# Optimization experiments

Measured on AMD Instinct MI355X. Metric: run time of the kernel, lower is better.

Reference implementation:

```python
import jax, jax.numpy as jnp
import numpy as np

DIM = 1024
B, S = 4, 4096

def setup_inputs() -> dict:
    key = jax.random.key(0)
    ks = jax.random.split(key, 8)
    scale = 1.0 / np.sqrt(DIM)
    x = jax.random.normal(ks[0], (B, S, DIM), dtype=jnp.float32)
    Wk = jax.random.normal(ks[1], (DIM, DIM), dtype=jnp.float32) * scale
    Wv = jax.random.normal(ks[2], (DIM, DIM), dtype=jnp.float32) * scale
    Wr = jax.random.normal(ks[3], (DIM, DIM), dtype=jnp.float32) * scale
    Wo = jax.random.normal(ks[4], (DIM, DIM), dtype=jnp.float32) * scale
    time_decay = jax.random.normal(ks[5], (DIM,), dtype=jnp.float32) * 0.01 - 5.0
    time_first = jax.random.normal(ks[6], (DIM,), dtype=jnp.float32) * 0.01
    return {"x": x, "Wk": Wk, "Wv": Wv, "Wr": Wr, "Wo": Wo,
            "time_decay": time_decay, "time_first": time_first}

def reference(x, Wk, Wv, Wr, Wo, time_decay, time_first):
    # Projections (Linear with weight [out, in]: y = x @ W^T)
    k = jnp.einsum('bsd,ed->bse', x, Wk)
    v = jnp.einsum('bsd,ed->bse', x, Wv)
    r = jax.nn.sigmoid(jnp.einsum('bsd,ed->bse', x, Wr))
    w = -jnp.exp(time_decay)          # (D,)
    decay = jnp.exp(w)                # exp(w), per-channel decay in (0,1)
    eu = jnp.exp(time_first)          # exp(u)
    kv = k * v                        # (B, S, D)

    def step(state, kv_t):
        wkv = state + eu * kv_t       # output numerator this step
        new_state = decay * state + kv_t
        return new_state, wkv

    state0 = jnp.zeros((x.shape[0], x.shape[2]), dtype=x.dtype)
    # scan over time axis: move S to leading dim
    _, wkv_seq = jax.lax.scan(step, state0, jnp.swapaxes(kv, 0, 1))  # (S, B, D)
    out = r * jnp.swapaxes(wkv_seq, 0, 1)  # (B, S, D)
    return jnp.einsum('bsd,ed->bse', out, Wo)
```

## Files before the change

kernel.cpp:

```cpp
#include <hip/hip_runtime.h>
#include <hip/hip_bf16.h>

#define DIMD   1024
#define BATCH  4
#define SEQ    4096
#define NTOK   (BATCH * SEQ)
#define CHUNK  64
#define NCHUNK (SEQ / CHUNK)

#define KBK    64
#define NKT    (DIMD / KBK)

typedef unsigned short ushort_t;
typedef __attribute__((ext_vector_type(8))) __bf16   bf16x8;
typedef __attribute__((ext_vector_type(4))) float    f32x4;
typedef __attribute__((ext_vector_type(8))) ushort_t u16x8;

__device__ __forceinline__ float b2f(ushort_t u) {
    union { unsigned int i; float f; } x;
    x.i = ((unsigned int)u) << 16;
    return x.f;
}

__device__ __forceinline__ ushort_t f2b(float f) {
    union { float f; unsigned int i; } x;
    x.f = f;
    unsigned int r = x.i + 0x7fffu + ((x.i >> 16) & 1u);
    return (ushort_t)(r >> 16);
}

#define GLL(gsrc, ldst) __builtin_amdgcn_global_load_lds( \
    (__attribute__((address_space(1))) void*)(gsrc), \
    (__attribute__((address_space(3))) void*)(ldst), 16, 0, 0)

__global__ __launch_bounds__(256)
void conv_f2b(const float* __restrict__ src, ushort_t* __restrict__ dst, int n8)
{
    const int i = blockIdx.x * 256 + threadIdx.x;
    if (i >= n8) return;
    const float4* s4 = (const float4*)src;
    const float4 a = s4[i * 2];
    const float4 b = s4[i * 2 + 1];
    u16x8 o;
    o[0] = f2b(a.x); o[1] = f2b(a.y); o[2] = f2b(a.z); o[3] = f2b(a.w);
    o[4] = f2b(b.x); o[5] = f2b(b.y); o[6] = f2b(b.z); o[7] = f2b(b.w);
    *(u16x8*)(dst + (size_t)i * 8) = o;
}

__global__ __launch_bounds__(256)
void conv_w(const float* __restrict__ W0, const float* __restrict__ W1,
            const float* __restrict__ W2, const float* __restrict__ W3,
            ushort_t* __restrict__ dst)
{
    const int m = blockIdx.y;
    const float* src = (m == 0) ? W0 : (m == 1) ? W1 : (m == 2) ? W2 : W3;
    const int i = blockIdx.x * 256 + threadIdx.x;
    const float4* s4 = (const float4*)src;
    const float4 a = s4[i * 2];
    const float4 b = s4[i * 2 + 1];
    u16x8 o;
    o[0] = f2b(a.x); o[1] = f2b(a.y); o[2] = f2b(a.z); o[3] = f2b(a.w);
    o[4] = f2b(b.x); o[5] = f2b(b.y); o[6] = f2b(b.z); o[7] = f2b(b.w);
    *(u16x8*)(dst + (size_t)m * DIMD * DIMD + (size_t)i * 8) = o;
}

__global__ __launch_bounds__(512, 2)
void gemm_kvr(const ushort_t* __restrict__ A,
              const ushort_t* __restrict__ Wk,
              const ushort_t* __restrict__ Wv,
              const ushort_t* __restrict__ Wr,
              const float* __restrict__ td,
              ushort_t* __restrict__ Okv,
              ushort_t* __restrict__ Or,
              float* __restrict__ cs)
{
    __shared__ __align__(16) ushort_t As[2][256 * KBK];
    __shared__ __align__(16) ushort_t Bk[2][64 * KBK];
    __shared__ __align__(16) ushort_t Bv[2][64 * KBK];
    __shared__ __align__(16) ushort_t Br[2][64 * KBK];

    const int tid  = threadIdx.x;
    const int lane = tid & 63;
    const int wv   = tid >> 6;
    const int wr   = wv >> 1;
    const int wc   = wv & 1;
    const int lrow = lane & 15;
    const int kq   = lane >> 4;
    const int s8   = lrow & 7;
    const int sw0  = (kq ^ s8) * 8;
    const int sw1  = ((kq + 4) ^ s8) * 8;

    const int row0 = blockIdx.x * 256;
    const int e0   = blockIdx.y * 64;

    const int r_  = tid >> 3;
    const int q_  = ((tid & 7) ^ (r_ & 7)) * 8;
    const size_t aoffs = (size_t)(row0 + r_) * DIMD + q_;
    const size_t boffs = (size_t)(e0 + r_) * DIMD + q_;

#define KVR_STAGE_A(dst, k0) do { \
    _Pragma("unroll") \
    for (int it_ = 0; it_ < 4; ++it_) \
        GLL(A + aoffs + (size_t)it_ * 64 * DIMD + (k0), \
            (char*)(dst) + (tid + it_ * 512) * 16); \
} while (0)

#define KVR_STAGE_B(dk, dv, dr, k0) do { \
    GLL(Wk + boffs + (k0), (char*)(dk) + tid * 16); \
    GLL(Wv + boffs + (k0), (char*)(dv) + tid * 16); \
    GLL(Wr + boffs + (k0), (char*)(dr) + tid * 16); \
} while (0)

    f32x4 ak[4][2], av[4][2], aR[4][2];
#pragma unroll
    for (int i = 0; i < 4; i++)
#pragma unroll
        for (int j = 0; j < 2; j++) {
            ak[i][j] = f32x4{0.f, 0.f, 0.f, 0.f};
            av[i][j] = f32x4{0.f, 0.f, 0.f, 0.f};
            aR[i][j] = f32x4{0.f, 0.f, 0.f, 0.f};
        }

    KVR_STAGE_A(&As[0][0], 0);
    KVR_STAGE_B(&Bk[0][0], &Bv[0][0], &Br[0][0], 0);
    asm volatile("" ::: "memory");
    KVR_STAGE_A(&As[1][0], KBK);
    asm volatile("s_waitcnt vmcnt(4)" ::: "memory");
    __builtin_amdgcn_s_barrier();

    auto tile = [&](int kt, ushort_t* Asb, ushort_t* Bkb, ushort_t* Bvb,
                    ushort_t* Brb, ushort_t* Bkn, ushort_t* Bvn, ushort_t* Brn) {
        bf16x8 af0[4], af1[4], b0[2], b1[2], c0[2], c1[2], d0[2], d1[2];

#pragma unroll
        for (int i = 0; i < 4; i++)
            af0[i] = *(const bf16x8*)(Asb + (wr * 64 + i * 16 + lrow) * KBK + sw0);
#pragma unroll
        for (int j = 0; j < 2; j++) {
            const int bo = (wc * 32 + j * 16 + lrow) * KBK + sw0;
            b0[j] = *(const bf16x8*)(Bkb + bo);
            c0[j] = *(const bf16x8*)(Bvb + bo);
        }
        if (kt + 1 < NKT) KVR_STAGE_B(Bkn, Bvn, Brn, (kt + 1) * KBK);
        __builtin_amdgcn_s_barrier();
        asm volatile("s_waitcnt lgkmcnt(0)" ::: "memory");
        __builtin_amdgcn_sched_barrier(0);
        __builtin_amdgcn_s_setprio(1);
#pragma unroll
        for (int i = 0; i < 4; i++)
#pragma unroll
            for (int j = 0; j < 2; j++) {
                ak[i][j] = __builtin_amdgcn_mfma_f32_16x16x32_bf16(af0[i], b0[j], ak[i][j], 0, 0, 0);
                av[i][j] = __builtin_amdgcn_mfma_f32_16x16x32_bf16(af0[i], c0[j], av[i][j], 0, 0, 0);
            }
        __builtin_amdgcn_s_setprio(0);
        __builtin_amdgcn_s_barrier();

#pragma unroll
        for (int j = 0; j < 2; j++)
            d0[j] = *(const bf16x8*)(Brb + (wc * 32 + j * 16 + lrow) * KBK + sw0);
#pragma unroll
        for (int i = 0; i < 4; i++)
            af1[i] = *(const bf16x8*)(Asb + (wr * 64 + i * 16 + lrow) * KBK + sw1);
        __builtin_amdgcn_s_barrier();
        asm volatile("s_waitcnt lgkmcnt(0)" ::: "memory");
        __builtin_amdgcn_sched_barrier(0);
        __builtin_amdgcn_s_setprio(1);
#pragma unroll
        for (int i = 0; i < 4; i++)
#pragma unroll
            for (int j = 0; j < 2; j++)
                aR[i][j] = __builtin_amdgcn_mfma_f32_16x16x32_bf16(af0[i], d0[j], aR[i][j], 0, 0, 0);
        __builtin_amdgcn_s_setprio(0);
        __builtin_amdgcn_s_barrier();

#pragma unroll
        for (int j = 0; j < 2; j++) {
            const int bo = (wc * 32 + j * 16 + lrow) * KBK + sw1;
            b1[j] = *(const bf16x8*)(Bkb + bo);
            c1[j] = *(const bf16x8*)(Bvb + bo);
        }
        if (kt + 2 < NKT) KVR_STAGE_A(Asb, (kt + 2) * KBK);
        __builtin_amdgcn_s_barrier();
        asm volatile("s_waitcnt lgkmcnt(0)" ::: "memory");
        __builtin_amdgcn_sched_barrier(0);
        __builtin_amdgcn_s_setprio(1);
#pragma unroll
        for (int i = 0; i < 4; i++)
#pragma unroll
            for (int j = 0; j < 2; j++) {
                ak[i][j] = __builtin_amdgcn_mfma_f32_16x16x32_bf16(af1[i], b1[j], ak[i][j], 0, 0, 0);
                av[i][j] = __builtin_amdgcn_mfma_f32_16x16x32_bf16(af1[i], c1[j], av[i][j], 0, 0, 0);
            }
        __builtin_amdgcn_s_setprio(0);
        __builtin_amdgcn_s_barrier();

#pragma unroll
        for (int j = 0; j < 2; j++)
            d1[j] = *(const bf16x8*)(Brb + (wc * 32 + j * 16 + lrow) * KBK + sw1);
        __builtin_amdgcn_s_barrier();
        asm volatile("s_waitcnt lgkmcnt(0)" ::: "memory");
        __builtin_amdgcn_sched_barrier(0);
        __builtin_amdgcn_s_setprio(1);
#pragma unroll
        for (int i = 0; i < 4; i++)
#pragma unroll
            for (int j = 0; j < 2; j++)
                aR[i][j] = __builtin_amdgcn_mfma_f32_16x16x32_bf16(af1[i], d1[j], aR[i][j], 0, 0, 0);
        __builtin_amdgcn_s_setprio(0);
        if (kt < NKT - 2)       asm volatile("s_waitcnt vmcnt(4)" ::: "memory");
        else if (kt == NKT - 2) asm volatile("s_waitcnt vmcnt(0)" ::: "memory");
        __builtin_amdgcn_s_barrier();
    };

    for (int m = 0; m < NKT / 2; ++m) {
        tile(2 * m,     &As[0][0], &Bk[0][0], &Bv[0][0], &Br[0][0],
                        &Bk[1][0], &Bv[1][0], &Br[1][0]);
        tile(2 * m + 1, &As[1][0], &Bk[1][0], &Bv[1][0], &Br[1][0],
                        &Bk[0][0], &Bv[0][0], &Br[0][0]);
    }

#pragma unroll
    for (int i = 0; i < 4; i++)
#pragma unroll
        for (int j = 0; j < 2; j++)
#pragma unroll
            for (int r = 0; r < 4; r++) {
                const int row = row0 + wr * 64 + i * 16 + kq * 4 + r;
                const int col = e0 + wc * 32 + j * 16 + lrow;
                const size_t o = (size_t)row * DIMD + col;
                Okv[o] = f2b(ak[i][j][r] * av[i][j][r]);
                Or[o]  = f2b(1.f / (1.f + __expf(-aR[i][j][r])));
            }

#pragma unroll
    for (int j = 0; j < 2; j++) {
        const int col = e0 + wc * 32 + j * 16 + lrow;
        const float w = -__expf(td[col]);
        float s = 0.f;
#pragma unroll
        for (int i = 0; i < 4; i++)
#pragma unroll
            for (int r = 0; r < 4; r++) {
                const int rl = i * 16 + kq * 4 + r;
                s += __expf(w * (float)(63 - rl)) * ak[i][j][r] * av[i][j][r];
            }
        s += __shfl_xor(s, 16);
        s += __shfl_xor(s, 32);
        if (kq == 0) {
            const int gchunk = (row0 >> 6) + wr;
            cs[(size_t)gchunk * DIMD + col] = s;
        }
    }
#undef KVR_STAGE_A
#undef KVR_STAGE_B
}

__global__ __launch_bounds__(512, 2)
void gemm_bt(const ushort_t* __restrict__ A,
             const ushort_t* __restrict__ W,
             float* __restrict__ Of)
{
    __shared__ __align__(16) ushort_t As[2][256 * KBK];
    __shared__ __align__(16) ushort_t Bs[2][256 * KBK];

    const int tid  = threadIdx.x;
    const int lane = tid & 63;
    const int wv   = tid >> 6;
    const int wr   = wv >> 2;
    const int wc   = wv & 3;
    const int lrow = lane & 15;
    const int kq   = lane >> 4;
    const int s8   = lrow & 7;
    const int sw0  = (kq ^ s8) * 8;
    const int sw1  = ((kq + 4) ^ s8) * 8;

    const int row0 = blockIdx.x * 256;
    const int e0   = blockIdx.y * 256;

    const int r_  = tid >> 3;
    const int q_  = ((tid & 7) ^ (r_ & 7)) * 8;
    const size_t aoffs = (size_t)(row0 + r_) * DIMD + q_;
    const size_t boffs = (size_t)(e0 + r_) * DIMD + q_;

#define BT_STAGE_A(dst, k0) do { \
    _Pragma("unroll") \
    for (int it_ = 0; it_ < 4; ++it_) \
        GLL(A + aoffs + (size_t)it_ * 64 * DIMD + (k0), \
            (char*)(dst) + (tid + it_ * 512) * 16); \
} while (0)

#define BT_STAGE_B(dst, k0) do { \
    _Pragma("unroll") \
    for (int it_ = 0; it_ < 4; ++it_) \
        GLL(W + boffs + (size_t)it_ * 64 * DIMD + (k0), \
            (char*)(dst) + (tid + it_ * 512) * 16); \
} while (0)

    f32x4 acc[8][4];
#pragma unroll
    for (int i = 0; i < 8; i++)
#pragma unroll
        for (int j = 0; j < 4; j++)
            acc[i][j] = f32x4{0.f, 0.f, 0.f, 0.f};

    BT_STAGE_A(&As[0][0], 0);
    BT_STAGE_B(&Bs[0][0], 0);
    asm volatile("" ::: "memory");
    BT_STAGE_A(&As[1][0], KBK);
    asm volatile("s_waitcnt vmcnt(4)" ::: "memory");
    __builtin_amdgcn_s_barrier();

    auto tile = [&](int kt, ushort_t* Asb, ushort_t* Bsb, ushort_t* Bsn) {
        bf16x8 af0[8], af1[8], bf0[4], bf1[4];

#pragma unroll
        for (int i = 0; i < 8; i++)
            af0[i] = *(const bf16x8*)(Asb + (wr * 128 + i * 16 + lrow) * KBK + sw0);
#pragma unroll
        for (int j = 0; j < 2; j++)
            bf0[j] = *(const bf16x8*)(Bsb + (wc * 64 + j * 16 + lrow) * KBK + sw0);
        if (kt + 1 < NKT) BT_STAGE_B(Bsn, (kt + 1) * KBK);
        __builtin_amdgcn_s_barrier();
        asm volatile("s_waitcnt lgkmcnt(0)" ::: "memory");
        __builtin_amdgcn_sched_barrier(0);
        __builtin_amdgcn_s_setprio(1);
#pragma unroll
        for (int i = 0; i < 8; i++)
#pragma unroll
            for (int j = 0; j < 2; j++)
                acc[i][j] = __builtin_amdgcn_mfma_f32_16x16x32_bf16(af0[i], bf0[j], acc[i][j], 0, 0, 0);
        __builtin_amdgcn_s_setprio(0);
        __builtin_amdgcn_s_barrier();

#pragma unroll
        for (int j = 2; j < 4; j++)
            bf0[j] = *(const bf16x8*)(Bsb + (wc * 64 + j * 16 + lrow) * KBK + sw0);
        __builtin_amdgcn_s_barrier();
        asm volatile("s_waitcnt lgkmcnt(0)" ::: "memory");
        __builtin_amdgcn_sched_barrier(0);
        __builtin_amdgcn_s_setprio(1);
#pragma unroll
        for (int i = 0; i < 8; i++)
#pragma unroll
            for (int j = 2; j < 4; j++)
                acc[i][j] = __builtin_amdgcn_mfma_f32_16x16x32_bf16(af0[i], bf0[j], acc[i][j], 0, 0, 0);
        __builtin_amdgcn_s_setprio(0);
        __builtin_amdgcn_s_barrier();

#pragma unroll
        for (int i = 0; i < 8; i++)
            af1[i] = *(const bf16x8*)(Asb + (wr * 128 + i * 16 + lrow) * KBK + sw1);
#pragma unroll
        for (int j = 0; j < 2; j++)
            bf1[j] = *(const bf16x8*)(Bsb + (wc * 64 + j * 16 + lrow) * KBK + sw1);
        __builtin_amdgcn_s_barrier();
        asm volatile("s_waitcnt lgkmcnt(0)" ::: "memory");
        __builtin_amdgcn_sched_barrier(0);
        __builtin_amdgcn_s_setprio(1);
#pragma unroll
        for (int i = 0; i < 8; i++)
#pragma unroll
            for (int j = 0; j < 2; j++)
                acc[i][j] = __builtin_amdgcn_mfma_f32_16x16x32_bf16(af1[i], bf1[j], acc[i][j], 0, 0, 0);
        __builtin_amdgcn_s_setprio(0);
        __builtin_amdgcn_s_barrier();

#pragma unroll
        for (int j = 2; j < 4; j++)
            bf1[j] = *(const bf16x8*)(Bsb + (wc * 64 + j * 16 + lrow) * KBK + sw1);
        if (kt + 2 < NKT) BT_STAGE_A(Asb, (kt + 2) * KBK);
        __builtin_amdgcn_s_barrier();
        asm volatile("s_waitcnt lgkmcnt(0)" ::: "memory");
        __builtin_amdgcn_sched_barrier(0);
        __builtin_amdgcn_s_setprio(1);
#pragma unroll
        for (int i = 0; i < 8; i++)
#pragma unroll
            for (int j = 2; j < 4; j++)
                acc[i][j] = __builtin_amdgcn_mfma_f32_16x16x32_bf16(af1[i], bf1[j], acc[i][j], 0, 0, 0);
        __builtin_amdgcn_s_setprio(0);
        if (kt < NKT - 2)       asm volatile("s_waitcnt vmcnt(4)" ::: "memory");
        else if (kt == NKT - 2) asm volatile("s_waitcnt vmcnt(0)" ::: "memory");
        __builtin_amdgcn_s_barrier();
    };

    for (int m = 0; m < NKT / 2; ++m) {
        tile(2 * m,     &As[0][0], &Bs[0][0], &Bs[1][0]);
        tile(2 * m + 1, &As[1][0], &Bs[1][0], &Bs[0][0]);
    }

#pragma unroll
    for (int i = 0; i < 8; i++)
#pragma unroll
        for (int j = 0; j < 4; j++)
#pragma unroll
            for (int r = 0; r < 4; r++) {
                const int row = row0 + wr * 128 + i * 16 + kq * 4 + r;
                const int col = e0 + wc * 64 + j * 16 + lrow;
                Of[(size_t)row * DIMD + col] = acc[i][j][r];
            }
#undef BT_STAGE_A
#undef BT_STAGE_B
}

__global__ __launch_bounds__(64)
void chunk_scan(float* __restrict__ cs, const float* __restrict__ td)
{
    const int idx = blockIdx.x * 64 + threadIdx.x;
    const int d = idx & (DIMD - 1);
    const int b = idx >> 10;

    const float w      = -__expf(td[d]);
    const float decayL = __expf(w * (float)CHUNK);

    float v[NCHUNK];
    const size_t base = ((size_t)b * NCHUNK) * DIMD + d;
#pragma unroll
    for (int c = 0; c < NCHUNK; c++)
        v[c] = cs[base + (size_t)c * DIMD];

    float st = 0.f;
#pragma unroll
    for (int c = 0; c < NCHUNK; c++) {
        const float sc = v[c];
        v[c] = st;
        st = decayL * st + sc;
    }

#pragma unroll
    for (int c = 0; c < NCHUNK; c++)
        cs[base + (size_t)c * DIMD] = v[c];
}

__global__ __launch_bounds__(64)
void emit(const ushort_t* __restrict__ kvb, const ushort_t* __restrict__ rb,
          const float* __restrict__ td, const float* __restrict__ tf,
          const float* __restrict__ cs, ushort_t* __restrict__ op)
{
    const int t  = blockIdx.x * 64 + threadIdx.x;
    const int d0 = (t & (DIMD / 8 - 1)) * 8;
    const int bc = t >> 7;
    const int c  = bc & (NCHUNK - 1);
    const int b  = bc >> 6;

    float decay[8], eu[8], st[8];
#pragma unroll
    for (int j = 0; j < 8; j++) {
        decay[j] = __expf(-__expf(td[d0 + j]));
        eu[j]    = __expf(tf[d0 + j]);
    }
    const float* csp = cs + ((size_t)bc * DIMD + d0);
    const float4 s0 = *(const float4*)csp;
    const float4 s1 = *(const float4*)(csp + 4);
    st[0] = s0.x; st[1] = s0.y; st[2] = s0.z; st[3] = s0.w;
    st[4] = s1.x; st[5] = s1.y; st[6] = s1.z; st[7] = s1.w;

    size_t off = ((size_t)b * SEQ + (size_t)c * CHUNK) * DIMD + d0;
#pragma unroll 8
    for (int i = 0; i < CHUNK; i++) {
        const u16x8 kv8 = *(const u16x8*)(kvb + off);
        const u16x8 r8  = *(const u16x8*)(rb + off);
        u16x8 o8;
#pragma unroll
        for (int j = 0; j < 8; j++) {
            const float kv = b2f(kv8[j]);
            o8[j] = f2b(b2f(r8[j]) * (st[j] + eu[j] * kv));
            st[j] = decay[j] * st[j] + kv;
        }
        *(u16x8*)(op + off) = o8;
        off += DIMD;
    }
}

extern "C" void kernel_launch(void* const* d_in, const int* in_sizes, int n_in,
                              void* d_out, int out_size, void* d_ws, size_t ws_size,
                              hipStream_t stream)
{
    const float* x  = (const float*)d_in[0];
    const float* Wk = (const float*)d_in[1];
    const float* Wv = (const float*)d_in[2];
    const float* Wr = (const float*)d_in[3];
    const float* Wo = (const float*)d_in[4];
    const float* td = (const float*)d_in[5];
    const float* tf = (const float*)d_in[6];

    ushort_t* xb  = (ushort_t*)d_ws;
    ushort_t* Wb  = xb + (size_t)NTOK * DIMD;
    ushort_t* Wkb = Wb;
    ushort_t* Wvb = Wb + (size_t)DIMD * DIMD;
    ushort_t* Wrb = Wb + 2 * (size_t)DIMD * DIMD;
    ushort_t* Wob = Wb + 3 * (size_t)DIMD * DIMD;
    float*    cs  = (float*)(Wb + 4 * (size_t)DIMD * DIMD);
    ushort_t* pbuf = xb;

    ushort_t* kvb = (ushort_t*)d_out;
    ushort_t* rb  = kvb + (size_t)NTOK * DIMD;
    float*    out = (float*)d_out;

    conv_f2b<<<NTOK * DIMD / 8 / 256, 256, 0, stream>>>(x, xb, NTOK * DIMD / 8);
    conv_w<<<dim3(DIMD * DIMD / 8 / 256, 4), 256, 0, stream>>>(Wk, Wv, Wr, Wo, Wb);

    gemm_kvr<<<dim3(NTOK / 256, DIMD / 64), 512, 0, stream>>>(
        xb, Wkb, Wvb, Wrb, td, kvb, rb, cs);

    chunk_scan<<<BATCH * DIMD / 64, 64, 0, stream>>>(cs, td);

    emit<<<BATCH * NCHUNK * (DIMD / 8) / 64, 64, 0, stream>>>(
        kvb, rb, td, tf, cs, pbuf);

    gemm_bt<<<dim3(NTOK / 256, DIMD / 256), 512, 0, stream>>>(pbuf, Wob, out);
}
```

Measured before the change: 309.4 us.

## Split fused KVR GEMM into wider KV GEMM and separate sigmoid R GEMM

The single K/V/R projection kernel with 64-wide output tiles is split in two. A K·V kernel uses 128-wide output tiles, which improves reuse of the A tile loaded into shared memory. A separate 256x256-tile GEMM computes sigmoid(x·Wr). Both aim at higher arithmetic intensity per loaded A tile. In exchange, x is read from memory twice more in total and there is one extra kernel launch.

```diff
diff --git a/kernel.cpp b/kernel.cpp
--- a/kernel.cpp
+++ b/kernel.cpp
@@ -65,19 +65,16 @@
 }
 
 __global__ __launch_bounds__(512, 2)
-void gemm_kvr(const ushort_t* __restrict__ A,
-              const ushort_t* __restrict__ Wk,
-              const ushort_t* __restrict__ Wv,
-              const ushort_t* __restrict__ Wr,
-              const float* __restrict__ td,
-              ushort_t* __restrict__ Okv,
-              ushort_t* __restrict__ Or,
-              float* __restrict__ cs)
+void gemm_kv(const ushort_t* __restrict__ A,
+             const ushort_t* __restrict__ Wk,
+             const ushort_t* __restrict__ Wv,
+             const float* __restrict__ td,
+             ushort_t* __restrict__ Okv,
+             float* __restrict__ cs)
 {
     __shared__ __align__(16) ushort_t As[2][256 * KBK];
-    __shared__ __align__(16) ushort_t Bk[2][64 * KBK];
-    __shared__ __align__(16) ushort_t Bv[2][64 * KBK];
-    __shared__ __align__(16) ushort_t Br[2][64 * KBK];
+    __shared__ __align__(16) ushort_t Bk[2][128 * KBK];
+    __shared__ __align__(16) ushort_t Bv[2][128 * KBK];
 
     const int tid  = threadIdx.x;
     const int lane = tid & 63;
@@ -91,57 +88,55 @@
     const int sw1  = ((kq + 4) ^ s8) * 8;
 
     const int row0 = blockIdx.x * 256;
-    const int e0   = blockIdx.y * 64;
+    const int e0   = blockIdx.y * 128;
 
     const int r_  = tid >> 3;
     const int q_  = ((tid & 7) ^ (r_ & 7)) * 8;
     const size_t aoffs = (size_t)(row0 + r_) * DIMD + q_;
     const size_t boffs = (size_t)(e0 + r_) * DIMD + q_;
 
-#define KVR_STAGE_A(dst, k0) do { \
+#define KV_STAGE_A(dst, k0) do { \
     _Pragma("unroll") \
     for (int it_ = 0; it_ < 4; ++it_) \
         GLL(A + aoffs + (size_t)it_ * 64 * DIMD + (k0), \
             (char*)(dst) + (tid + it_ * 512) * 16); \
 } while (0)
 
-#define KVR_STAGE_B(dk, dv, dr, k0) do { \
-    GLL(Wk + boffs + (k0), (char*)(dk) + tid * 16); \
-    GLL(Wv + boffs + (k0), (char*)(dv) + tid * 16); \
-    GLL(Wr + boffs + (k0), (char*)(dr) + tid * 16); \
+#define KV_STAGE_B(Wp, dst, k0) do { \
+    _Pragma("unroll") \
+    for (int it_ = 0; it_ < 2; ++it_) \
+        GLL((Wp) + boffs + (size_t)it_ * 64 * DIMD + (k0), \
+            (char*)(dst) + (tid + it_ * 512) * 16); \
 } while (0)
 
-    f32x4 ak[4][2], av[4][2], aR[4][2];
+    f32x4 ak[4][4], av[4][4];
 #pragma unroll
     for (int i = 0; i < 4; i++)
 #pragma unroll
-        for (int j = 0; j < 2; j++) {
+        for (int j = 0; j < 4; j++) {
             ak[i][j] = f32x4{0.f, 0.f, 0.f, 0.f};
             av[i][j] = f32x4{0.f, 0.f, 0.f, 0.f};
-            aR[i][j] = f32x4{0.f, 0.f, 0.f, 0.f};
         }
 
-    KVR_STAGE_A(&As[0][0], 0);
-    KVR_STAGE_B(&Bk[0][0], &Bv[0][0], &Br[0][0], 0);
+    KV_STAGE_A(&As[0][0], 0);
+    KV_STAGE_B(Wk, &Bk[0][0], 0);
+    KV_STAGE_B(Wv, &Bv[0][0], 0);
     asm volatile("" ::: "memory");
-    KVR_STAGE_A(&As[1][0], KBK);
+    KV_STAGE_A(&As[1][0], KBK);
     asm volatile("s_waitcnt vmcnt(4)" ::: "memory");
     __builtin_amdgcn_s_barrier();
 
     auto tile = [&](int kt, ushort_t* Asb, ushort_t* Bkb, ushort_t* Bvb,
-                    ushort_t* Brb, ushort_t* Bkn, ushort_t* Bvn, ushort_t* Brn) {
-        bf16x8 af0[4], af1[4], b0[2], b1[2], c0[2], c1[2], d0[2], d1[2];
+                    ushort_t* Bkn, ushort_t* Bvn) {
+        bf16x8 af0[4], af1[4], b0[4], b1[4], c0[4], c1[4];
 
 #pragma unroll
         for (int i = 0; i < 4; i++)
             af0[i] = *(const bf16x8*)(Asb + (wr * 64 + i * 16 + lrow) * KBK + sw0);
 #pragma unroll
-        for (int j = 0; j < 2; j++) {
-            const int bo = (wc * 32 + j * 16 + lrow) * KBK + sw0;
-            b0[j] = *(const bf16x8*)(Bkb + bo);
-            c0[j] = *(const bf16x8*)(Bvb + bo);
-        }
-        if (kt + 1 < NKT) KVR_STAGE_B(Bkn, Bvn, Brn, (kt + 1) * KBK);
+        for (int j = 0; j < 4; j++)
+            b0[j] = *(const bf16x8*)(Bkb + (wc * 64 + j * 16 + lrow) * KBK + sw0);
+        if (kt + 1 < NKT) KV_STAGE_B(Wk, Bkn, (kt + 1) * KBK);
         __builtin_amdgcn_s_barrier();
         asm volatile("s_waitcnt lgkmcnt(0)" ::: "memory");
         __builtin_amdgcn_sched_barrier(0);
@@ -149,19 +144,33 @@
 #pragma unroll
         for (int i = 0; i < 4; i++)
 #pragma unroll
-            for (int j = 0; j < 2; j++) {
+            for (int j = 0; j < 4; j++)
                 ak[i][j] = __builtin_amdgcn_mfma_f32_16x16x32_bf16(af0[i], b0[j], ak[i][j], 0, 0, 0);
+        __builtin_amdgcn_s_setprio(0);
+        __builtin_amdgcn_s_barrier();
+
+#pragma unroll
+        for (int j = 0; j < 4; j++)
+            c0[j] = *(const bf16x8*)(Bvb + (wc * 64 + j * 16 + lrow) * KBK + sw0);
+        if (kt + 1 < NKT) KV_STAGE_B(Wv, Bvn, (kt + 1) * KBK);
+        __builtin_amdgcn_s_barrier();
+        asm volatile("s_waitcnt lgkmcnt(0)" ::: "memory");
+        __builtin_amdgcn_sched_barrier(0);
+        __builtin_amdgcn_s_setprio(1);
+#pragma unroll
+        for (int i = 0; i < 4; i++)
+#pragma unroll
+            for (int j = 0; j < 4; j++)
                 av[i][j] = __builtin_amdgcn_mfma_f32_16x16x32_bf16(af0[i], c0[j], av[i][j], 0, 0, 0);
-            }
-        __builtin_amdgcn_s_setprio(0);
-        __builtin_amdgcn_s_barrier();
-
-#pragma unroll
-        for (int j = 0; j < 2; j++)
-            d0[j] = *(const bf16x8*)(Brb + (wc * 32 + j * 16 + lrow) * KBK + sw0);
+        __builtin_amdgcn_s_setprio(0);
+        __builtin_amdgcn_s_barrier();
+
 #pragma unroll
         for (int i = 0; i < 4; i++)
             af1[i] = *(const bf16x8*)(Asb + (wr * 64 + i * 16 + lrow) * KBK + sw1);
+#pragma unroll
+        for (int j = 0; j < 4; j++)
+            b1[j] = *(const bf16x8*)(Bkb + (wc * 64 + j * 16 + lrow) * KBK + sw1);
         __builtin_amdgcn_s_barrier();
         asm volatile("s_waitcnt lgkmcnt(0)" ::: "memory");
         __builtin_amdgcn_sched_barrier(0);
@@ -169,18 +178,15 @@
 #pragma unroll
         for (int i = 0; i < 4; i++)
 #pragma unroll
-            for (int j = 0; j < 2; j++)
-                aR[i][j] = __builtin_amdgcn_mfma_f32_16x16x32_bf16(af0[i], d0[j], aR[i][j], 0, 0, 0);
-        __builtin_amdgcn_s_setprio(0);
-        __builtin_amdgcn_s_barrier();
-
-#pragma unroll
-        for (int j = 0; j < 2; j++) {
-            const int bo = (wc * 32 + j * 16 + lrow) * KBK + sw1;
-            b1[j] = *(const bf16x8*)(Bkb + bo);
-            c1[j] = *(const bf16x8*)(Bvb + bo);
-        }
-        if (kt + 2 < NKT) KVR_STAGE_A(Asb, (kt + 2) * KBK);
+            for (int j = 0; j < 4; j++)
+                ak[i][j] = __builtin_amdgcn_mfma_f32_16x16x32_bf16(af1[i], b1[j], ak[i][j], 0, 0, 0);
+        __builtin_amdgcn_s_setprio(0);
+        __builtin_amdgcn_s_barrier();
+
+#pragma unroll
+        for (int j = 0; j < 4; j++)
+            c1[j] = *(const bf16x8*)(Bvb + (wc * 64 + j * 16 + lrow) * KBK + sw1);
+        if (kt + 2 < NKT) KV_STAGE_A(Asb, (kt + 2) * KBK);
         __builtin_amdgcn_s_barrier();
         asm volatile("s_waitcnt lgkmcnt(0)" ::: "memory");
         __builtin_amdgcn_sched_barrier(0);
@@ -188,25 +194,8 @@
 #pragma unroll
         for (int i = 0; i < 4; i++)
 #pragma unroll
-            for (int j = 0; j < 2; j++) {
-                ak[i][j] = __builtin_amdgcn_mfma_f32_16x16x32_bf16(af1[i], b1[j], ak[i][j], 0, 0, 0);
+            for (int j = 0; j < 4; j++)
                 av[i][j] = __builtin_amdgcn_mfma_f32_16x16x32_bf16(af1[i], c1[j], av[i][j], 0, 0, 0);
-            }
-        __builtin_amdgcn_s_setprio(0);
-        __builtin_amdgcn_s_barrier();
-
-#pragma unroll
-        for (int j = 0; j < 2; j++)
-            d1[j] = *(const bf16x8*)(Brb + (wc * 32 + j * 16 + lrow) * KBK + sw1);
-        __builtin_amdgcn_s_barrier();
-        asm volatile("s_waitcnt lgkmcnt(0)" ::: "memory");
-        __builtin_amdgcn_sched_barrier(0);
-        __builtin_amdgcn_s_setprio(1);
-#pragma unroll
-        for (int i = 0; i < 4; i++)
-#pragma unroll
-            for (int j = 0; j < 2; j++)
-                aR[i][j] = __builtin_amdgcn_mfma_f32_16x16x32_bf16(af1[i], d1[j], aR[i][j], 0, 0, 0);
         __builtin_amdgcn_s_setprio(0);
         if (kt < NKT - 2)       asm volatile("s_waitcnt vmcnt(4)" ::: "memory");
         else if (kt == NKT - 2) asm volatile("s_waitcnt vmcnt(0)" ::: "memory");
@@ -214,28 +203,24 @@
     };
 
     for (int m = 0; m < NKT / 2; ++m) {
-        tile(2 * m,     &As[0][0], &Bk[0][0], &Bv[0][0], &Br[0][0],
-                        &Bk[1][0], &Bv[1][0], &Br[1][0]);
-        tile(2 * m + 1, &As[1][0], &Bk[1][0], &Bv[1][0], &Br[1][0],
-                        &Bk[0][0], &Bv[0][0], &Br[0][0]);
+        tile(2 * m,     &As[0][0], &Bk[0][0], &Bv[0][0], &Bk[1][0], &Bv[1][0]);
+        tile(2 * m + 1, &As[1][0], &Bk[1][0], &Bv[1][0], &Bk[0][0], &Bv[0][0]);
     }
 
 #pragma unroll
     for (int i = 0; i < 4; i++)
 #pragma unroll
-        for (int j = 0; j < 2; j++)
+        for (int j = 0; j < 4; j++)
 #pragma unroll
             for (int r = 0; r < 4; r++) {
                 const int row = row0 + wr * 64 + i * 16 + kq * 4 + r;
-                const int col = e0 + wc * 32 + j * 16 + lrow;
-                const size_t o = (size_t)row * DIMD + col;
-                Okv[o] = f2b(ak[i][j][r] * av[i][j][r]);
-                Or[o]  = f2b(1.f / (1.f + __expf(-aR[i][j][r])));
+                const int col = e0 + wc * 64 + j * 16 + lrow;
+                Okv[(size_t)row * DIMD + col] = f2b(ak[i][j][r] * av[i][j][r]);
             }
 
 #pragma unroll
-    for (int j = 0; j < 2; j++) {
-        const int col = e0 + wc * 32 + j * 16 + lrow;
+    for (int j = 0; j < 4; j++) {
+        const int col = e0 + wc * 64 + j * 16 + lrow;
         const float w = -__expf(td[col]);
         float s = 0.f;
 #pragma unroll
@@ -252,14 +237,14 @@
             cs[(size_t)gchunk * DIMD + col] = s;
         }
     }
-#undef KVR_STAGE_A
-#undef KVR_STAGE_B
+#undef KV_STAGE_A
+#undef KV_STAGE_B
 }
 
 __global__ __launch_bounds__(512, 2)
-void gemm_bt(const ushort_t* __restrict__ A,
+void gemm_rs(const ushort_t* __restrict__ A,
              const ushort_t* __restrict__ W,
-             float* __restrict__ Of)
+             ushort_t* __restrict__ Or)
 {
     __shared__ __align__(16) ushort_t As[2][256 * KBK];
     __shared__ __align__(16) ushort_t Bs[2][256 * KBK];
@@ -283,6 +268,155 @@
     const size_t aoffs = (size_t)(row0 + r_) * DIMD + q_;
     const size_t boffs = (size_t)(e0 + r_) * DIMD + q_;
 
+#define RS_STAGE_A(dst, k0) do { \
+    _Pragma("unroll") \
+    for (int it_ = 0; it_ < 4; ++it_) \
+        GLL(A + aoffs + (size_t)it_ * 64 * DIMD + (k0), \
+            (char*)(dst) + (tid + it_ * 512) * 16); \
+} while (0)
+
+#define RS_STAGE_B(dst, k0) do { \
+    _Pragma("unroll") \
+    for (int it_ = 0; it_ < 4; ++it_) \
+        GLL(W + boffs + (size_t)it_ * 64 * DIMD + (k0), \
+            (char*)(dst) + (tid + it_ * 512) * 16); \
+} while (0)
+
+    f32x4 acc[8][4];
+#pragma unroll
+    for (int i = 0; i < 8; i++)
+#pragma unroll
+        for (int j = 0; j < 4; j++)
+            acc[i][j] = f32x4{0.f, 0.f, 0.f, 0.f};
+
+    RS_STAGE_A(&As[0][0], 0);
+    RS_STAGE_B(&Bs[0][0], 0);
+    asm volatile("" ::: "memory");
+    RS_STAGE_A(&As[1][0], KBK);
+    asm volatile("s_waitcnt vmcnt(4)" ::: "memory");
+    __builtin_amdgcn_s_barrier();
+
+    auto tile = [&](int kt, ushort_t* Asb, ushort_t* Bsb, ushort_t* Bsn) {
+        bf16x8 af0[8], af1[8], bf0[4], bf1[4];
+
+#pragma unroll
+        for (int i = 0; i < 8; i++)
+            af0[i] = *(const bf16x8*)(Asb + (wr * 128 + i * 16 + lrow) * KBK + sw0);
+#pragma unroll
+        for (int j = 0; j < 2; j++)
+            bf0[j] = *(const bf16x8*)(Bsb + (wc * 64 + j * 16 + lrow) * KBK + sw0);
+        if (kt + 1 < NKT) RS_STAGE_B(Bsn, (kt + 1) * KBK);
+        __builtin_amdgcn_s_barrier();
+        asm volatile("s_waitcnt lgkmcnt(0)" ::: "memory");
+        __builtin_amdgcn_sched_barrier(0);
+        __builtin_amdgcn_s_setprio(1);
+#pragma unroll
+        for (int i = 0; i < 8; i++)
+#pragma unroll
+            for (int j = 0; j < 2; j++)
+                acc[i][j] = __builtin_amdgcn_mfma_f32_16x16x32_bf16(af0[i], bf0[j], acc[i][j], 0, 0, 0);
+        __builtin_amdgcn_s_setprio(0);
+        __builtin_amdgcn_s_barrier();
+
+#pragma unroll
+        for (int j = 2; j < 4; j++)
+            bf0[j] = *(const bf16x8*)(Bsb + (wc * 64 + j * 16 + lrow) * KBK + sw0);
+        __builtin_amdgcn_s_barrier();
+        asm volatile("s_waitcnt lgkmcnt(0)" ::: "memory");
+        __builtin_amdgcn_sched_barrier(0);
+        __builtin_amdgcn_s_setprio(1);
+#pragma unroll
+        for (int i = 0; i < 8; i++)
+#pragma unroll
+            for (int j = 2; j < 4; j++)
+                acc[i][j] = __builtin_amdgcn_mfma_f32_16x16x32_bf16(af0[i], bf0[j], acc[i][j], 0, 0, 0);
+        __builtin_amdgcn_s_setprio(0);
+        __builtin_amdgcn_s_barrier();
+
+#pragma unroll
+        for (int i = 0; i < 8; i++)
+            af1[i] = *(const bf16x8*)(Asb + (wr * 128 + i * 16 + lrow) * KBK + sw1);
+#pragma unroll
+        for (int j = 0; j < 2; j++)
+            bf1[j] = *(const bf16x8*)(Bsb + (wc * 64 + j * 16 + lrow) * KBK + sw1);
+        __builtin_amdgcn_s_barrier();
+        asm volatile("s_waitcnt lgkmcnt(0)" ::: "memory");
+        __builtin_amdgcn_sched_barrier(0);
+        __builtin_amdgcn_s_setprio(1);
+#pragma unroll
+        for (int i = 0; i < 8; i++)
+#pragma unroll
+            for (int j = 0; j < 2; j++)
+                acc[i][j] = __builtin_amdgcn_mfma_f32_16x16x32_bf16(af1[i], bf1[j], acc[i][j], 0, 0, 0);
+        __builtin_amdgcn_s_setprio(0);
+        __builtin_amdgcn_s_barrier();
+
+#pragma unroll
+        for (int j = 2; j < 4; j++)
+            bf1[j] = *(const bf16x8*)(Bsb + (wc * 64 + j * 16 + lrow) * KBK + sw1);
+        if (kt + 2 < NKT) RS_STAGE_A(Asb, (kt + 2) * KBK);
+        __builtin_amdgcn_s_barrier();
+        asm volatile("s_waitcnt lgkmcnt(0)" ::: "memory");
+        __builtin_amdgcn_sched_barrier(0);
+        __builtin_amdgcn_s_setprio(1);
+#pragma unroll
+        for (int i = 0; i < 8; i++)
+#pragma unroll
+            for (int j = 2; j < 4; j++)
+                acc[i][j] = __builtin_amdgcn_mfma_f32_16x16x32_bf16(af1[i], bf1[j], acc[i][j], 0, 0, 0);
+        __builtin_amdgcn_s_setprio(0);
+        if (kt < NKT - 2)       asm volatile("s_waitcnt vmcnt(4)" ::: "memory");
+        else if (kt == NKT - 2) asm volatile("s_waitcnt vmcnt(0)" ::: "memory");
+        __builtin_amdgcn_s_barrier();
+    };
+
+    for (int m = 0; m < NKT / 2; ++m) {
+        tile(2 * m,     &As[0][0], &Bs[0][0], &Bs[1][0]);
+        tile(2 * m + 1, &As[1][0], &Bs[1][0], &Bs[0][0]);
+    }
+
+#pragma unroll
+    for (int i = 0; i < 8; i++)
+#pragma unroll
+        for (int j = 0; j < 4; j++)
+#pragma unroll
+            for (int r = 0; r < 4; r++) {
+                const int row = row0 + wr * 128 + i * 16 + kq * 4 + r;
+                const int col = e0 + wc * 64 + j * 16 + lrow;
+                Or[(size_t)row * DIMD + col] =
+                    f2b(1.f / (1.f + __expf(-acc[i][j][r])));
+            }
+#undef RS_STAGE_A
+#undef RS_STAGE_B
+}
+
+__global__ __launch_bounds__(512, 2)
+void gemm_bt(const ushort_t* __restrict__ A,
+             const ushort_t* __restrict__ W,
+             float* __restrict__ Of)
+{
+    __shared__ __align__(16) ushort_t As[2][256 * KBK];
+    __shared__ __align__(16) ushort_t Bs[2][256 * KBK];
+
+    const int tid  = threadIdx.x;
+    const int lane = tid & 63;
+    const int wv   = tid >> 6;
+    const int wr   = wv >> 2;
+    const int wc   = wv & 3;
+    const int lrow = lane & 15;
+    const int kq   = lane >> 4;
+    const int s8   = lrow & 7;
+    const int sw0  = (kq ^ s8) * 8;
+    const int sw1  = ((kq + 4) ^ s8) * 8;
+
+    const int row0 = blockIdx.x * 256;
+    const int e0   = blockIdx.y * 256;
+
+    const int r_  = tid >> 3;
+    const int q_  = ((tid & 7) ^ (r_ & 7)) * 8;
+    const size_t aoffs = (size_t)(row0 + r_) * DIMD + q_;
+    const size_t boffs = (size_t)(e0 + r_) * DIMD + q_;
+
 #define BT_STAGE_A(dst, k0) do { \
     _Pragma("unroll") \
     for (int it_ = 0; it_ < 4; ++it_) \
@@ -501,8 +635,10 @@
     conv_f2b<<<NTOK * DIMD / 8 / 256, 256, 0, stream>>>(x, xb, NTOK * DIMD / 8);
     conv_w<<<dim3(DIMD * DIMD / 8 / 256, 4), 256, 0, stream>>>(Wk, Wv, Wr, Wo, Wb);
 
-    gemm_kvr<<<dim3(NTOK / 256, DIMD / 64), 512, 0, stream>>>(
-        xb, Wkb, Wvb, Wrb, td, kvb, rb, cs);
+    gemm_kv<<<dim3(NTOK / 256, DIMD / 128), 512, 0, stream>>>(
+        xb, Wkb, Wvb, td, kvb, cs);
+
+    gemm_rs<<<dim3(NTOK / 256, DIMD / 256), 512, 0, stream>>>(xb, Wrb, rb);
 
     chunk_scan<<<BATCH * DIMD / 64, 64, 0, stream>>>(cs, td);
 
```

Result: no change. 308.5 us (-0.3%).
